# Optimization experiments

Measured on AMD Instinct MI355X. Metric: run time of the kernel, lower is better.

The kernel has to match this reference:

```python
import jax, jax.numpy as jnp
import numpy as np

N_NODES = 256


def _lstm_layer(x, W, b):
    # x: [B, T, D]; W: [D+H, 4H]; b: [4H]. TF BasicLSTMCell, forget_bias=1.0,
    # gate order (i, j, f, o).
    B, T, D = x.shape
    H = N_NODES

    def step(carry, xt):
        c, h = carry
        gates = jnp.dot(jnp.concatenate([xt, h], axis=1), W) + b  # [B, 4H]
        i, j, f, o = jnp.split(gates, 4, axis=1)
        c_new = c * jax.nn.sigmoid(f + 1.0) + jax.nn.sigmoid(i) * jnp.tanh(j)
        h_new = jnp.tanh(c_new) * jax.nn.sigmoid(o)
        return (c_new, h_new), h_new

    init = (jnp.zeros((B, H), x.dtype), jnp.zeros((B, H), x.dtype))
    _, ys = jax.lax.scan(step, init, jnp.swapaxes(x, 0, 1))  # ys: [T, B, H]
    return jnp.swapaxes(ys, 0, 1)


def setup_inputs() -> dict:
    key = jax.random.key(0)
    k_x, k_w0, k_w1 = jax.random.split(key, 3)
    B, T, D, H = 32, 2048, 256, N_NODES
    x = jax.random.normal(k_x, (B, T, D), dtype=jnp.float32)
    W0 = jax.random.normal(k_w0, (D + H, 4 * H), dtype=jnp.float32) * 0.05
    b0 = jnp.zeros((4 * H,), dtype=jnp.float32)
    W1 = jax.random.normal(k_w1, (H + H, 4 * H), dtype=jnp.float32) * 0.05
    b1 = jnp.zeros((4 * H,), dtype=jnp.float32)
    return {"x": x, "W0": W0, "b0": b0, "W1": W1, "b1": b1}


def reference(x, W0, b0, W1, b1):
    # 2-layer LSTM stack, zero initial states, keepProb=1.0 (no dropout).
    h = _lstm_layer(x, W0, b0)
    h = _lstm_layer(h, W1, b1)
    # activations = reshape(outputs, [-1, nNodes * numCells]), numCells = 1
    return h.reshape(-1, N_NODES)
```

## Files before the change

### kernel.cpp

```cpp
#include <hip/hip_runtime.h>
#include <hip/hip_bf16.h>
#include <hip/hip_fp16.h>


typedef _Float16 half_t;
typedef __attribute__((ext_vector_type(2))) _Float16 h2v;

static __device__ __forceinline__ float bf2f(unsigned short u) {
  union { unsigned u; float f; } v; v.u = ((unsigned)u) << 16; return v.f;
}
static __device__ __forceinline__ unsigned short f2bf(float f) {
  union { float f; unsigned u; } v; v.f = f;
  unsigned r = v.u + 0x7fffu + ((v.u >> 16) & 1u);
  return (unsigned short)(r >> 16);
}
static __device__ __forceinline__ float ldw(const void* p, long i, int fp32) {
  return fp32 ? ((const float*)p)[i] : bf2f(((const unsigned short*)p)[i]);
}
static __device__ __forceinline__ unsigned short f16b(float f) {
  return __builtin_bit_cast(unsigned short, (half_t)f);
}
static __device__ __forceinline__ h2v BC(unsigned u) {
  return __builtin_bit_cast(h2v, u);
}
static __device__ __forceinline__ float rcpf(float x) { return __builtin_amdgcn_rcpf(x); }
static __device__ __forceinline__ float sigm(float x) { return rcpf(1.f + __expf(-x)); }
static __device__ __forceinline__ float tanh_(float x) {
  float e = __expf(-2.f * fabsf(x));
  float t = (1.f - e) * rcpf(1.f + e);
  return copysignf(t, x);
}
static __device__ __forceinline__ float fdot2(h2v a, h2v b, float c) {
#if __has_builtin(__builtin_amdgcn_fdot2)
  return __builtin_amdgcn_fdot2(a, b, c, false);
#else
  return c + (float)a.x * (float)b.x + (float)a.y * (float)b.y;
#endif
}

__global__ __launch_bounds__(256) void detect(const unsigned short* __restrict__ x,
                                              int* __restrict__ flag) {
  __shared__ int cnt;
  if (threadIdx.x == 0) cnt = 0;
  __syncthreads();
  int c = 0;
#pragma unroll
  for (int i = 0; i < 8; ++i) {
    unsigned short u = x[threadIdx.x * 8 + i];
    c += (((u >> 7) & 0xFF) >= 192) ? 1 : 0;
  }
  atomicAdd(&cnt, c);
  __syncthreads();
  if (threadIdx.x == 0) *flag = (cnt > 16) ? 1 : 0;
}

__global__ __launch_bounds__(256) void prep(
    const void* __restrict__ W0, const void* __restrict__ W1,
    const void* __restrict__ b0, const void* __restrict__ b1,
    const int* __restrict__ dtf,
    unsigned* __restrict__ Wrec, float* __restrict__ bias0,
    float* __restrict__ bias1)
{
  const int fp32 = *dtf;
  int id = blockIdx.x * 256 + threadIdx.x;
  if (blockIdx.y == 0) {
    int i  = id & 127;
    int tid = (id >> 7) & 511;
    int sL = id >> 16;
    int L = sL >> 2, s = sL & 3;
    int kq = tid >> 8, c = tid & 255;
    int col = ((c >> 6) << 8) + s * 64 + (c & 63);
    long r0 = (long)(kq * 256 + 2 * i) * 1024 + col;
    const void* W = L ? W1 : W0;
    unsigned lo = f16b(ldw(W, r0, fp32));
    unsigned hi = f16b(ldw(W, r0 + 1024, fp32));
    Wrec[id] = lo | (hi << 16);
  } else {
    if (id < 1024)       bias0[id] = ldw(b0, id, fp32);
    else if (id < 2048)  bias1[id - 1024] = ldw(b1, id - 1024, fp32);
  }
}

__global__ __launch_bounds__(512) void recur(
    const void* __restrict__ x, const unsigned* __restrict__ Wrec,
    const float* __restrict__ bias0, const float* __restrict__ bias1,
    unsigned* H1T, unsigned* H2R,
    void* __restrict__ dout, const int* __restrict__ dtf)
{
  const int fp32 = *dtf;
  const int bi = blockIdx.x;
  const int L = bi >> 7, sL = bi >> 5, s = sL & 3, b = bi & 31;
  const int tid = threadIdx.x;
  const int kq = tid >> 8, c = tid & 255;
  const int hbase = kq << 5;

  __shared__ __align__(16) unsigned short hbufh[512];
  __shared__ float part[2][256];
  __shared__ float bg[256];

  const uint4* wp4 = (const uint4*)Wrec + ((size_t)sL * 512 + tid) * 32;
  uint4 w00 = wp4[0],  w01 = wp4[1],  w02 = wp4[2],  w03 = wp4[3];
  uint4 w04 = wp4[4],  w05 = wp4[5],  w06 = wp4[6],  w07 = wp4[7];
  uint4 w08 = wp4[8],  w09 = wp4[9],  w10 = wp4[10], w11 = wp4[11];
  uint4 w12 = wp4[12], w13 = wp4[13], w14 = wp4[14], w15 = wp4[15];
  uint4 w16 = wp4[16], w17 = wp4[17], w18 = wp4[18], w19 = wp4[19];
  uint4 w20 = wp4[20], w21 = wp4[21], w22 = wp4[22], w23 = wp4[23];
  uint4 w24 = wp4[24], w25 = wp4[25], w26 = wp4[26], w27 = wp4[27];
  uint4 w28 = wp4[28], w29 = wp4[29], w30 = wp4[30], w31 = wp4[31];

  if (tid < 256) {
    int scol = ((c >> 6) << 8) + s * 64 + (c & 63);
    bg[c] = (L ? bias1 : bias0)[scol];
  }

  const uint4* hbufu4 = (const uint4*)hbufh;
  float cst = 0.f;

  for (int t = 0; t < 2048; ++t) {
    const int t1 = t - 1;
    if (!L) {
      if (tid < 256) {
        size_t xi = ((size_t)b * 2048 + t) * 256 + tid;
        float xv = fp32 ? ((const float*)x)[xi]
                        : bf2f(((const unsigned short*)x)[xi]);
        hbufh[tid] = f16b(xv);
      } else if (t == 0) {
        hbufh[tid] = 0;
      } else {
        const unsigned* pw = H1T + ((size_t)t1 * 32 + b) * 256 + (tid - 256);
        unsigned v;
        do { v = __hip_atomic_load(pw, __ATOMIC_RELAXED,
                                   __HIP_MEMORY_SCOPE_AGENT); }
        while ((v >> 16) != (unsigned)t1);
        hbufh[tid] = (unsigned short)v;
      }
    } else {
      if (tid < 256) {
        const unsigned* pw = H1T + ((size_t)t * 32 + b) * 256 + tid;
        unsigned v;
        do { v = __hip_atomic_load(pw, __ATOMIC_RELAXED,
                                   __HIP_MEMORY_SCOPE_AGENT); }
        while ((v >> 16) != (unsigned)t);
        hbufh[tid] = (unsigned short)v;
      } else if (t == 0) {
        hbufh[tid] = 0;
      } else {
        const unsigned* pw = H2R + ((size_t)(t1 & 3) * 32 + b) * 256 + (tid - 256);
        unsigned v;
        do { v = __hip_atomic_load(pw, __ATOMIC_RELAXED,
                                   __HIP_MEMORY_SCOPE_AGENT); }
        while ((v >> 16) != (unsigned)t1);
        hbufh[tid] = (unsigned short)v;
      }
    }
    __syncthreads();

    float a0 = 0.f, a1 = 0.f, a2 = 0.f, a3 = 0.f;
#define STEPW(W_, I_) { uint4 hv = hbufu4[hbase + I_];      \
    a0 = fdot2(BC(hv.x), BC(W_.x), a0);                     \
    a1 = fdot2(BC(hv.y), BC(W_.y), a1);                     \
    a2 = fdot2(BC(hv.z), BC(W_.z), a2);                     \
    a3 = fdot2(BC(hv.w), BC(W_.w), a3); }
    STEPW(w00, 0)  STEPW(w01, 1)  STEPW(w02, 2)  STEPW(w03, 3)
    STEPW(w04, 4)  STEPW(w05, 5)  STEPW(w06, 6)  STEPW(w07, 7)
    STEPW(w08, 8)  STEPW(w09, 9)  STEPW(w10, 10) STEPW(w11, 11)
    STEPW(w12, 12) STEPW(w13, 13) STEPW(w14, 14) STEPW(w15, 15)
    STEPW(w16, 16) STEPW(w17, 17) STEPW(w18, 18) STEPW(w19, 19)
    STEPW(w20, 20) STEPW(w21, 21) STEPW(w22, 22) STEPW(w23, 23)
    STEPW(w24, 24) STEPW(w25, 25) STEPW(w26, 26) STEPW(w27, 27)
    STEPW(w28, 28) STEPW(w29, 29) STEPW(w30, 30) STEPW(w31, 31)
#undef STEPW
    part[kq][c] = (a0 + a1) + (a2 + a3);
    __syncthreads();

    if (tid < 64) {
      int j = tid;
      float gi = part[0][j]       + part[1][j]       + bg[j];
      float gj = part[0][64 + j]  + part[1][64 + j]  + bg[64 + j];
      float gf = part[0][128 + j] + part[1][128 + j] + bg[128 + j];
      float go = part[0][192 + j] + part[1][192 + j] + bg[192 + j];
      float cn = cst * sigm(gf + 1.f) + sigm(gi) * tanh_(gj);
      cst = cn;
      float h = tanh_(cn) * sigm(go);
      unsigned val = ((unsigned)t << 16) | (unsigned)f16b(h);
      if (!L) {
        __hip_atomic_store(H1T + ((size_t)t * 32 + b) * 256 + s * 64 + j, val,
                           __ATOMIC_RELAXED, __HIP_MEMORY_SCOPE_AGENT);
      } else {
        __hip_atomic_store(H2R + ((size_t)(t & 3) * 32 + b) * 256 + s * 64 + j,
                           val, __ATOMIC_RELAXED, __HIP_MEMORY_SCOPE_AGENT);
        size_t oi = ((size_t)b * 2048 + t) * 256 + s * 64 + j;
        if (fp32) ((float*)dout)[oi] = h;
        else      ((unsigned short*)dout)[oi] = f2bf(h);
      }
    }
  }
}

extern "C" void kernel_launch(void* const* d_in, const int* in_sizes, int n_in,
                              void* d_out, int out_size, void* d_ws, size_t ws_size,
                              hipStream_t stream) {
  const void* x  = d_in[0];
  const void* W0 = d_in[1];
  const void* b0 = d_in[2];
  const void* W1 = d_in[3];
  const void* b1 = d_in[4];

  char* p = (char*)d_ws;
  unsigned* Wrec = (unsigned*)p; p += (size_t)524288 * 4;
  unsigned* H1T  = (unsigned*)p; p += (size_t)2048 * 32 * 256 * 4;
  unsigned* H2R  = (unsigned*)p; p += (size_t)4 * 32 * 256 * 4;
  float* bias0   = (float*)p;    p += 4096;
  float* bias1   = (float*)p;    p += 4096;
  int* dflag     = (int*)p;      p += 256;

  detect<<<1, 256, 0, stream>>>((const unsigned short*)x, dflag);
  prep<<<dim3(2048, 2), 256, 0, stream>>>(W0, W1, b0, b1, dflag,
                                          Wrec, bias0, bias1);
  recur<<<256, 512, 0, stream>>>(x, Wrec, bias0, bias1,
                                 H1T, H2R, d_out, dflag);
}
```

Baseline: 3.189 ms.

## Split gate dot product so input half overlaps polling for recurrent state

The K dimension is re-laid out so every thread handles half of the input rows and half of the recurrent rows. The input (or layer-0 output) half of the dot product now runs before the thread waits for the previous step's hidden state. The next step's input is staged into shared memory early, with x prefetched two steps ahead. Polling is also unrolled into batches of four atomic loads. The aim is to hide cross-block synchronisation latency behind useful compute, at the cost of extra barrier ordering complexity and more shared-buffer reuse hazards.

```diff
diff --git a/kernel.cpp b/kernel.cpp
--- a/kernel.cpp
+++ b/kernel.cpp
@@ -36,6 +36,23 @@
 #else
   return c + (float)a.x * (float)b.x + (float)a.y * (float)b.y;
 #endif
+}
+static __device__ __forceinline__ unsigned ald(const unsigned* p) {
+  return __hip_atomic_load(p, __ATOMIC_RELAXED, __HIP_MEMORY_SCOPE_AGENT);
+}
+static __device__ __forceinline__ unsigned poll_tag(const unsigned* p, unsigned tg) {
+  unsigned v = ald(p);
+  while ((v >> 16) != tg) {
+    unsigned a = ald(p);
+    unsigned b = ald(p);
+    unsigned c = ald(p);
+    unsigned d = ald(p);
+    if ((a >> 16) == tg) { v = a; break; }
+    if ((b >> 16) == tg) { v = b; break; }
+    if ((c >> 16) == tg) { v = c; break; }
+    v = d;
+  }
+  return v;
 }
 
 __global__ __launch_bounds__(256) void detect(const unsigned short* __restrict__ x,
@@ -70,7 +87,8 @@
     int L = sL >> 2, s = sL & 3;
     int kq = tid >> 8, c = tid & 255;
     int col = ((c >> 6) << 8) + s * 64 + (c & 63);
-    long r0 = (long)(kq * 256 + 2 * i) * 1024 + col;
+    int p  = i >> 6, ii = i & 63;
+    long r0 = (long)(p * 256 + kq * 128 + 2 * ii) * 1024 + col;
     const void* W = L ? W1 : W0;
     unsigned lo = f16b(ldw(W, r0, fp32));
     unsigned hi = f16b(ldw(W, r0 + 1024, fp32));
@@ -92,7 +110,8 @@
   const int L = bi >> 7, sL = bi >> 5, s = sL & 3, b = bi & 31;
   const int tid = threadIdx.x;
   const int kq = tid >> 8, c = tid & 255;
-  const int hbase = kq << 5;
+  const int abase = kq << 4;
+  const int bbase = 32 + (kq << 4);
 
   __shared__ __align__(16) unsigned short hbufh[512];
   __shared__ float part[2][256];
@@ -116,61 +135,65 @@
   const uint4* hbufu4 = (const uint4*)hbufh;
   float cst = 0.f;
 
+  float xv = 0.f;
+  if (tid < 256) {
+    if (!L) {
+      size_t xi = (size_t)b * 2048 * 256 + tid;
+      hbufh[tid] = f16b(fp32 ? ((const float*)x)[xi]
+                             : bf2f(((const unsigned short*)x)[xi]));
+      size_t xj = xi + 256;
+      xv = fp32 ? ((const float*)x)[xj] : bf2f(((const unsigned short*)x)[xj]);
+    } else {
+      unsigned v = poll_tag(H1T + (size_t)b * 256 + tid, 0u);
+      hbufh[tid] = (unsigned short)v;
+    }
+  } else {
+    hbufh[tid] = 0;
+  }
+  __syncthreads();
+
   for (int t = 0; t < 2048; ++t) {
-    const int t1 = t - 1;
-    if (!L) {
-      if (tid < 256) {
-        size_t xi = ((size_t)b * 2048 + t) * 256 + tid;
-        float xv = fp32 ? ((const float*)x)[xi]
-                        : bf2f(((const unsigned short*)x)[xi]);
+    float a0 = 0.f, a1 = 0.f, a2 = 0.f, a3 = 0.f;
+#define STEPD(BASE_, W_, J_) { uint4 hv = hbufu4[BASE_ + J_];  \
+    a0 = fdot2(BC(hv.x), BC(W_.x), a0);                        \
+    a1 = fdot2(BC(hv.y), BC(W_.y), a1);                        \
+    a2 = fdot2(BC(hv.z), BC(W_.z), a2);                        \
+    a3 = fdot2(BC(hv.w), BC(W_.w), a3); }
+    STEPD(abase, w00, 0)  STEPD(abase, w01, 1)  STEPD(abase, w02, 2)  STEPD(abase, w03, 3)
+    STEPD(abase, w04, 4)  STEPD(abase, w05, 5)  STEPD(abase, w06, 6)  STEPD(abase, w07, 7)
+    STEPD(abase, w08, 8)  STEPD(abase, w09, 9)  STEPD(abase, w10, 10) STEPD(abase, w11, 11)
+    STEPD(abase, w12, 12) STEPD(abase, w13, 13) STEPD(abase, w14, 14) STEPD(abase, w15, 15)
+
+    if (t > 0 && tid >= 256) {
+      const unsigned tg = (unsigned)(t - 1);
+      const unsigned* pw = L
+        ? H2R + ((size_t)((t - 1) & 3) * 32 + b) * 256 + (tid - 256)
+        : H1T + ((size_t)(t - 1) * 32 + b) * 256 + (tid - 256);
+      hbufh[tid] = (unsigned short)poll_tag(pw, tg);
+    }
+    __syncthreads();
+
+    STEPD(bbase, w16, 0)  STEPD(bbase, w17, 1)  STEPD(bbase, w18, 2)  STEPD(bbase, w19, 3)
+    STEPD(bbase, w20, 4)  STEPD(bbase, w21, 5)  STEPD(bbase, w22, 6)  STEPD(bbase, w23, 7)
+    STEPD(bbase, w24, 8)  STEPD(bbase, w25, 9)  STEPD(bbase, w26, 10) STEPD(bbase, w27, 11)
+    STEPD(bbase, w28, 12) STEPD(bbase, w29, 13) STEPD(bbase, w30, 14) STEPD(bbase, w31, 15)
+#undef STEPD
+    part[kq][c] = (a0 + a1) + (a2 + a3);
+
+    if (t < 2047 && tid < 256) {
+      if (!L) {
         hbufh[tid] = f16b(xv);
-      } else if (t == 0) {
-        hbufh[tid] = 0;
+        if (t + 2 < 2048) {
+          size_t xi = ((size_t)b * 2048 + (t + 2)) * 256 + tid;
+          xv = fp32 ? ((const float*)x)[xi]
+                    : bf2f(((const unsigned short*)x)[xi]);
+        }
       } else {
-        const unsigned* pw = H1T + ((size_t)t1 * 32 + b) * 256 + (tid - 256);
-        unsigned v;
-        do { v = __hip_atomic_load(pw, __ATOMIC_RELAXED,
-                                   __HIP_MEMORY_SCOPE_AGENT); }
-        while ((v >> 16) != (unsigned)t1);
+        unsigned v = poll_tag(H1T + ((size_t)(t + 1) * 32 + b) * 256 + tid,
+                              (unsigned)(t + 1));
         hbufh[tid] = (unsigned short)v;
       }
-    } else {
-      if (tid < 256) {
-        const unsigned* pw = H1T + ((size_t)t * 32 + b) * 256 + tid;
-        unsigned v;
-        do { v = __hip_atomic_load(pw, __ATOMIC_RELAXED,
-                                   __HIP_MEMORY_SCOPE_AGENT); }
-        while ((v >> 16) != (unsigned)t);
-        hbufh[tid] = (unsigned short)v;
-      } else if (t == 0) {
-        hbufh[tid] = 0;
-      } else {
-        const unsigned* pw = H2R + ((size_t)(t1 & 3) * 32 + b) * 256 + (tid - 256);
-        unsigned v;
-        do { v = __hip_atomic_load(pw, __ATOMIC_RELAXED,
-                                   __HIP_MEMORY_SCOPE_AGENT); }
-        while ((v >> 16) != (unsigned)t1);
-        hbufh[tid] = (unsigned short)v;
-      }
-    }
-    __syncthreads();
-
-    float a0 = 0.f, a1 = 0.f, a2 = 0.f, a3 = 0.f;
-#define STEPW(W_, I_) { uint4 hv = hbufu4[hbase + I_];      \
-    a0 = fdot2(BC(hv.x), BC(W_.x), a0);                     \
-    a1 = fdot2(BC(hv.y), BC(W_.y), a1);                     \
-    a2 = fdot2(BC(hv.z), BC(W_.z), a2);                     \
-    a3 = fdot2(BC(hv.w), BC(W_.w), a3); }
-    STEPW(w00, 0)  STEPW(w01, 1)  STEPW(w02, 2)  STEPW(w03, 3)
-    STEPW(w04, 4)  STEPW(w05, 5)  STEPW(w06, 6)  STEPW(w07, 7)
-    STEPW(w08, 8)  STEPW(w09, 9)  STEPW(w10, 10) STEPW(w11, 11)
-    STEPW(w12, 12) STEPW(w13, 13) STEPW(w14, 14) STEPW(w15, 15)
-    STEPW(w16, 16) STEPW(w17, 17) STEPW(w18, 18) STEPW(w19, 19)
-    STEPW(w20, 20) STEPW(w21, 21) STEPW(w22, 22) STEPW(w23, 23)
-    STEPW(w24, 24) STEPW(w25, 25) STEPW(w26, 26) STEPW(w27, 27)
-    STEPW(w28, 28) STEPW(w29, 29) STEPW(w30, 30) STEPW(w31, 31)
-#undef STEPW
-    part[kq][c] = (a0 + a1) + (a2 + a3);
+    }
     __syncthreads();
 
     if (tid < 64) {
```

New measurement: 3.176 ms. No clear change (-0.4%).
